# Performance work log

Measured on AMD Instinct MI355X. Metric: run time of the kernel, lower is better.

The kernel has to match this reference:

```python
import jax, jax.numpy as jnp
import numpy as np

NUM_HEAD = 12
D_MODEL = 768
SEQ_LEN = 4096
D_K = D_MODEL // NUM_HEAD
NEG = -1e9  # matches masked_fill(-1000000000.0)


def setup_inputs() -> dict:
    key = jax.random.key(0)
    ks = jax.random.split(key, 9)
    s = 1.0 / np.sqrt(D_MODEL)
    inp = {
        "x": jax.random.normal(ks[0], (1, SEQ_LEN, D_MODEL), jnp.float32),
        "Wq": jax.random.normal(ks[1], (D_MODEL, D_MODEL), jnp.float32) * s,
        "bq": jax.random.normal(ks[2], (D_MODEL,), jnp.float32) * 0.01,
        "Wk": jax.random.normal(ks[3], (D_MODEL, D_MODEL), jnp.float32) * s,
        "bk": jax.random.normal(ks[4], (D_MODEL,), jnp.float32) * 0.01,
        "Wv": jax.random.normal(ks[5], (D_MODEL, D_MODEL), jnp.float32) * s,
        "bv": jax.random.normal(ks[6], (D_MODEL,), jnp.float32) * 0.01,
        "Wo": jax.random.normal(ks[7], (D_MODEL, D_MODEL), jnp.float32) * s,
        "bo": jax.random.normal(ks[8], (D_MODEL,), jnp.float32) * 0.01,
    }
    return inp


def reference(x, Wq, bq, Wk, bk, Wv, bv, Wo, bo):
    # x: [B, S, D]. nn.Linear computes x @ W.T + b.
    B, S, D = x.shape

    def proj(W, b):
        y = jnp.einsum("bsd,ed->bse", x, W) + b
        # [B, S, H, d_k] -> [B, H, S, d_k]
        return y.reshape(B, S, NUM_HEAD, D_K).transpose(0, 2, 1, 3)

    q = proj(Wq, bq)
    k = proj(Wk, bk)
    v = proj(Wv, bv)

    scores = jnp.einsum("bhqd,bhkd->bhqk", q, k) / jnp.sqrt(
        jnp.asarray(D_K, x.dtype)
    )
    # causal (subsequent) mask: position q attends to k <= q
    causal = jnp.tril(jnp.ones((S, S), bool))
    scores = jnp.where(causal[None, None], scores, jnp.asarray(NEG, x.dtype))
    p_attn = jax.nn.softmax(scores, axis=-1)  # dropout is identity in eval
    ctx = jnp.einsum("bhqk,bhkd->bhqd", p_attn, v)
    ctx = ctx.transpose(0, 2, 1, 3).reshape(B, S, D)
    return jnp.einsum("bsd,ed->bse", ctx, Wo) + bo
```

## Files before the change

### kernel.cpp

```cpp
#include <hip/hip_runtime.h>

#define SEQ 4096
#define DM  768
#define NH  12
#define DK  64

typedef __bf16 bf16_t;
typedef bf16_t bf16x8 __attribute__((ext_vector_type(8)));
typedef bf16_t bf16x4 __attribute__((ext_vector_type(4)));
typedef float  f32x4  __attribute__((ext_vector_type(4)));
typedef short  s16x4  __attribute__((ext_vector_type(4)));

#define LOG2E 1.44269504088896340736f
#define SM_C  16.0f

static __device__ inline f32x4 mfma16x16x16_bf16(bf16x4 a, bf16x4 b, f32x4 c) {
#if __has_builtin(__builtin_amdgcn_mfma_f32_16x16x16_bf16)
    return __builtin_amdgcn_mfma_f32_16x16x16_bf16(a, b, c, 0, 0, 0);
#else
    return __builtin_amdgcn_mfma_f32_16x16x16bf16_1k(
        __builtin_bit_cast(s16x4, a), __builtin_bit_cast(s16x4, b), c, 0, 0, 0);
#endif
}

static __device__ __forceinline__ void gl_lds16(const bf16_t* g, bf16_t* l) {
    __builtin_amdgcn_global_load_lds(
        (const __attribute__((address_space(1))) void*)g,
        (__attribute__((address_space(3))) void*)l, 16, 0, 0);
}

__global__ __launch_bounds__(256) void cvt_bf16(
    const float* __restrict__ x,  const float* __restrict__ Wq,
    const float* __restrict__ Wk, const float* __restrict__ Wv,
    const float* __restrict__ Wo,
    bf16_t* __restrict__ xb, bf16_t* __restrict__ Wb)
{
    const int NXV = SEQ * DM / 4;
    const int NWV = DM * DM / 4;
    int i4 = blockIdx.x * 256 + threadIdx.x;
    const float* src; bf16_t* dst; int off;
    if (i4 < NXV) { src = x; dst = xb; off = i4; }
    else {
        int j = i4 - NXV;
        int w = j / NWV, jj = j - w * NWV;
        src = (w == 0) ? Wq : (w == 1) ? Wk : (w == 2) ? Wv : Wo;
        dst = Wb + (size_t)w * DM * DM;
        off = jj;
    }
    float4 v = *(const float4*)&src[(size_t)off * 4];
    bf16x4 t;
    t[0] = (bf16_t)v.x; t[1] = (bf16_t)v.y; t[2] = (bf16_t)v.z; t[3] = (bf16_t)v.w;
    *(bf16x4*)&dst[(size_t)off * 4] = t;
}

__global__ __launch_bounds__(256) void gemm_qkv2(
    const bf16_t* __restrict__ A, const bf16_t* __restrict__ Wb,
    const float* __restrict__ bq, const float* __restrict__ bk,
    const float* __restrict__ bv,
    bf16_t* __restrict__ Qb, bf16_t* __restrict__ Kb, bf16_t* __restrict__ Vbt)
{
    const int z = blockIdx.z;
    const bf16_t* W = Wb + (size_t)z * DM * DM;
    const float* bias = (z == 0) ? bq : (z == 1) ? bk : bv;

    __shared__ bf16_t As[128][64];
    __shared__ bf16_t Bs[128][64];

    const int tid  = threadIdx.x;
    const int wave = tid >> 6;
    const int lane = tid & 63;
    const int wm   = wave & 1, wn = wave >> 1;
    const int lrow = lane & 15;
    const int quad = lane >> 4;
    const int row0 = blockIdx.x * 128;
    const int col0 = blockIdx.y * 128;

    const int srow   = lane >> 3;
    const int schunk = (lane & 7) ^ srow;
    const int swz    = lrow & 7;

    f32x4 acc[4][4];
    #pragma unroll
    for (int i = 0; i < 4; i++)
        #pragma unroll
        for (int j = 0; j < 4; j++)
            acc[i][j] = (f32x4){0.f, 0.f, 0.f, 0.f};

    for (int k0 = 0; k0 < DM; k0 += 64) {
        __syncthreads();
        #pragma unroll
        for (int u = 0; u < 4; u++) {
            int R0 = wave * 32 + u * 8;
            gl_lds16(&A[(size_t)(row0 + R0 + srow) * DM + k0 + schunk * 8],
                     &As[R0][0]);
            gl_lds16(&W[(size_t)(col0 + R0 + srow) * DM + k0 + schunk * 8],
                     &Bs[R0][0]);
        }
        __syncthreads();

        #pragma unroll
        for (int s = 0; s < 2; s++) {
            bf16x8 af[4], bfr[4];
            #pragma unroll
            for (int mt = 0; mt < 4; mt++)
                af[mt] = *(const bf16x8*)
                    &As[wm * 64 + mt * 16 + lrow][(((s << 2) | quad) ^ swz) * 8];
            #pragma unroll
            for (int nt = 0; nt < 4; nt++)
                bfr[nt] = *(const bf16x8*)
                    &Bs[wn * 64 + nt * 16 + lrow][(((s << 2) | quad) ^ swz) * 8];
            #pragma unroll
            for (int mt = 0; mt < 4; mt++)
                #pragma unroll
                for (int nt = 0; nt < 4; nt++)
                    acc[mt][nt] = __builtin_amdgcn_mfma_f32_16x16x32_bf16(
                        af[mt], bfr[nt], acc[mt][nt], 0, 0, 0);
        }
    }

    if (z == 2) {
        #pragma unroll
        for (int nt = 0; nt < 4; nt++) {
            int col = col0 + wn * 64 + nt * 16 + lrow;
            float bvv = bias[col];
            #pragma unroll
            for (int mt = 0; mt < 4; mt++) {
                int row = row0 + wm * 64 + mt * 16 + quad * 4;
                bf16x4 t;
                #pragma unroll
                for (int r = 0; r < 4; r++) t[r] = (bf16_t)(acc[mt][nt][r] + bvv);
                *(bf16x4*)&Vbt[(size_t)col * SEQ + row] = t;
            }
        }
    } else {
        bf16_t* Cout = (z == 0) ? Qb : Kb;
        float scale = (z == 1) ? 0.125f : 1.0f;
        #pragma unroll
        for (int nt = 0; nt < 4; nt++) {
            int col = col0 + wn * 64 + nt * 16 + lrow;
            float bvv = bias[col];
            #pragma unroll
            for (int mt = 0; mt < 4; mt++) {
                #pragma unroll
                for (int r = 0; r < 4; r++) {
                    int row = row0 + wm * 64 + mt * 16 + quad * 4 + r;
                    Cout[(size_t)row * DM + col] =
                        (bf16_t)((acc[mt][nt][r] + bvv) * scale);
                }
            }
        }
    }
}

__global__ __launch_bounds__(256) void gemm_out2(
    const bf16_t* __restrict__ A, const bf16_t* __restrict__ W,
    const float* __restrict__ bias, float* __restrict__ C)
{
    __shared__ bf16_t As[128][64];
    __shared__ bf16_t Bs[64][64];

    const int tid  = threadIdx.x;
    const int wave = tid >> 6;
    const int lane = tid & 63;
    const int wm   = wave & 1, wn = wave >> 1;
    const int lrow = lane & 15;
    const int quad = lane >> 4;
    const int row0 = blockIdx.x * 128;
    const int col0 = blockIdx.y * 64;

    const int srow   = lane >> 3;
    const int schunk = (lane & 7) ^ srow;
    const int swz    = lrow & 7;

    f32x4 acc[4][2];
    #pragma unroll
    for (int i = 0; i < 4; i++)
        #pragma unroll
        for (int j = 0; j < 2; j++)
            acc[i][j] = (f32x4){0.f, 0.f, 0.f, 0.f};

    for (int k0 = 0; k0 < DM; k0 += 64) {
        __syncthreads();
        #pragma unroll
        for (int u = 0; u < 4; u++) {
            int R0 = wave * 32 + u * 8;
            gl_lds16(&A[(size_t)(row0 + R0 + srow) * DM + k0 + schunk * 8],
                     &As[R0][0]);
        }
        #pragma unroll
        for (int u = 0; u < 2; u++) {
            int R0 = wave * 16 + u * 8;
            gl_lds16(&W[(size_t)(col0 + R0 + srow) * DM + k0 + schunk * 8],
                     &Bs[R0][0]);
        }
        __syncthreads();

        #pragma unroll
        for (int s = 0; s < 2; s++) {
            bf16x8 af[4], bfr[2];
            #pragma unroll
            for (int mt = 0; mt < 4; mt++)
                af[mt] = *(const bf16x8*)
                    &As[wm * 64 + mt * 16 + lrow][(((s << 2) | quad) ^ swz) * 8];
            #pragma unroll
            for (int nt = 0; nt < 2; nt++)
                bfr[nt] = *(const bf16x8*)
                    &Bs[wn * 32 + nt * 16 + lrow][(((s << 2) | quad) ^ swz) * 8];
            #pragma unroll
            for (int mt = 0; mt < 4; mt++)
                #pragma unroll
                for (int nt = 0; nt < 2; nt++)
                    acc[mt][nt] = __builtin_amdgcn_mfma_f32_16x16x32_bf16(
                        af[mt], bfr[nt], acc[mt][nt], 0, 0, 0);
        }
    }

    #pragma unroll
    for (int nt = 0; nt < 2; nt++) {
        int col = col0 + wn * 32 + nt * 16 + lrow;
        float bvv = bias[col];
        #pragma unroll
        for (int mt = 0; mt < 4; mt++) {
            #pragma unroll
            for (int r = 0; r < 4; r++) {
                int row = row0 + wm * 64 + mt * 16 + quad * 4 + r;
                C[(size_t)row * DM + col] = acc[mt][nt][r] + bvv;
            }
        }
    }
}

__global__ __launch_bounds__(256) void flash_split2(
    const bf16_t* __restrict__ Qb, const bf16_t* __restrict__ Kb,
    const bf16_t* __restrict__ Vbt,
    float* __restrict__ Oacc ,
    float* __restrict__ Lacc )
{
    const int qi = blockIdx.x;
    const int s0 = blockIdx.y * 16;
    if (s0 > qi) return;
    const int h    = blockIdx.z;
    const int kend = min(s0 + 15, qi);
    const int tid  = threadIdx.x;
    const int wave = tid >> 6;
    const int lane = tid & 63;
    const int lrow = lane & 15;
    const int quad = lane >> 4;
    const int q0   = qi * 64;

    __shared__ bf16_t Ks[2][64][72];
    __shared__ bf16_t Vt[2][64][76];

    const int qrow = q0 + wave * 16 + lrow;
    bf16x8 qfrag[2];
    #pragma unroll
    for (int s = 0; s < 2; s++)
        qfrag[s] = *(const bf16x8*)&Qb[(size_t)qrow * DM + h * DK + s * 32 + quad * 8];

    f32x4 oT[4];
    #pragma unroll
    for (int dt = 0; dt < 4; dt++) oT[dt] = (f32x4){0.f, 0.f, 0.f, 0.f};
    float l_i = 0.f;

    const int r0 = tid >> 3;
    const int c0 = (tid & 7) * 8;
    const bf16_t* Kbase = Kb  + (size_t)h * DK + c0;
    const bf16_t* Vbase = Vbt + (size_t)(h * DK) * SEQ + c0;

    size_t ko = (size_t)s0 * 64;
    bf16x8 kr0 = *(const bf16x8*)&Kbase[(ko + r0)      * DM];
    bf16x8 kr1 = *(const bf16x8*)&Kbase[(ko + r0 + 32) * DM];
    bf16x8 vr0 = *(const bf16x8*)&Vbase[(size_t)(r0)      * SEQ + ko];
    bf16x8 vr1 = *(const bf16x8*)&Vbase[(size_t)(r0 + 32) * SEQ + ko];

    for (int kt = s0; kt <= kend; kt++) {
        const int b = kt & 1;
        *(bf16x8*)&Ks[b][r0][c0]      = kr0;
        *(bf16x8*)&Ks[b][r0 + 32][c0] = kr1;
        *(bf16x8*)&Vt[b][r0][c0]      = vr0;
        *(bf16x8*)&Vt[b][r0 + 32][c0] = vr1;
        __syncthreads();

        if (kt < kend) {
            size_t kn = (size_t)(kt + 1) * 64;
            kr0 = *(const bf16x8*)&Kbase[(kn + r0)      * DM];
            kr1 = *(const bf16x8*)&Kbase[(kn + r0 + 32) * DM];
            vr0 = *(const bf16x8*)&Vbase[(size_t)(r0)      * SEQ + kn];
            vr1 = *(const bf16x8*)&Vbase[(size_t)(r0 + 32) * SEQ + kn];
        }

        f32x4 sc[4];
        #pragma unroll
        for (int mt = 0; mt < 4; mt++) {
            f32x4 a = (f32x4){0.f, 0.f, 0.f, 0.f};
            #pragma unroll
            for (int s = 0; s < 2; s++) {
                bf16x8 kf = *(const bf16x8*)&Ks[b][mt * 16 + lrow][s * 32 + quad * 8];
                a = __builtin_amdgcn_mfma_f32_16x16x32_bf16(kf, qfrag[s], a, 0, 0, 0);
            }
            sc[mt] = a;
        }

        if (kt == qi) {
            int lq = wave * 16 + lrow;
            #pragma unroll
            for (int mt = 0; mt < 4; mt++)
                #pragma unroll
                for (int r = 0; r < 4; r++)
                    if (mt * 16 + quad * 4 + r > lq) sc[mt][r] = -1e30f;
        }

        bf16x4 pf[4];
        float rsum = 0.f;
        #pragma unroll
        for (int mt = 0; mt < 4; mt++) {
            bf16x4 t;
            #pragma unroll
            for (int r = 0; r < 4; r++) {
                float p = __builtin_amdgcn_exp2f((sc[mt][r] - SM_C) * LOG2E);
                rsum += p;
                t[r] = (bf16_t)p;
            }
            pf[mt] = t;
        }
        l_i += rsum;

        #pragma unroll
        for (int dt = 0; dt < 4; dt++)
            #pragma unroll
            for (int kb = 0; kb < 4; kb++) {
                bf16x4 vf = *(const bf16x4*)&Vt[b][dt * 16 + lrow][kb * 16 + quad * 4];
                oT[dt] = mfma16x16x16_bf16(vf, pf[kb], oT[dt]);
            }
    }

    #pragma unroll
    for (int dt = 0; dt < 4; dt++)
        #pragma unroll
        for (int r = 0; r < 4; r++) {
            int d = dt * 16 + quad * 4 + r;
            atomicAdd(&Oacc[((size_t)h * DK + d) * SEQ + q0 + wave * 16 + lrow],
                      oT[dt][r]);
        }
    l_i += __shfl_xor(l_i, 16, 64);
    l_i += __shfl_xor(l_i, 32, 64);
    if (quad == 0)
        atomicAdd(&Lacc[(size_t)h * SEQ + qrow], l_i);
}

__global__ __launch_bounds__(256) void ctx_epilogue(
    const float* __restrict__ Oacc, const float* __restrict__ Lacc,
    bf16_t* __restrict__ Ctx)
{
    const int qt = blockIdx.x;
    const int h  = blockIdx.y;
    const int tid = threadIdx.x;
    __shared__ float T[64][65];

    #pragma unroll
    for (int i = 0; i < 4; i++) {
        int v  = tid + i * 256;
        int d  = v >> 4;
        int qv = v & 15;
        f32x4 o4 = *(const f32x4*)&Oacc[((size_t)h * DK + d) * SEQ + qt * 64 + qv * 4];
        f32x4 l4 = *(const f32x4*)&Lacc[(size_t)h * SEQ + qt * 64 + qv * 4];
        #pragma unroll
        for (int j = 0; j < 4; j++)
            T[qv * 4 + j][d] = o4[j] / l4[j];
    }
    __syncthreads();
    #pragma unroll
    for (int i = 0; i < 2; i++) {
        int v  = tid + i * 256;
        int q  = v >> 3;
        int c8 = v & 7;
        bf16x8 t;
        #pragma unroll
        for (int j = 0; j < 8; j++)
            t[j] = (bf16_t)T[q][c8 * 8 + j];
        *(bf16x8*)&Ctx[(size_t)(qt * 64 + q) * DM + h * DK + c8 * 8] = t;
    }
}

extern "C" void kernel_launch(void* const* d_in, const int* in_sizes, int n_in,
                              void* d_out, int out_size, void* d_ws, size_t ws_size,
                              hipStream_t stream) {
    const float* x  = (const float*)d_in[0];
    const float* Wq = (const float*)d_in[1];
    const float* bq = (const float*)d_in[2];
    const float* Wk = (const float*)d_in[3];
    const float* bk = (const float*)d_in[4];
    const float* Wv = (const float*)d_in[5];
    const float* bv = (const float*)d_in[6];
    const float* Wo = (const float*)d_in[7];
    const float* bo = (const float*)d_in[8];
    float* out = (float*)d_out;

    const size_t NX = (size_t)SEQ * DM;
    const size_t NW = (size_t)DM * DM;

    bf16_t* xb   = (bf16_t*)d_ws;
    bf16_t* Qb   = xb  + NX;
    bf16_t* Kb   = Qb  + NX;
    bf16_t* Vbt  = Kb  + NX;
    bf16_t* Wb   = Vbt + NX;
    float*  Oacc = (float*)(Wb + 4 * NW);
    float*  Lacc = Oacc + NX;
    bf16_t* Cx   = xb;

    int cvt_blocks = (int)((NX + 4 * NW) / 4 / 256);
    cvt_bf16<<<cvt_blocks, 256, 0, stream>>>(x, Wq, Wk, Wv, Wo, xb, Wb);
    hipMemsetAsync(Oacc, 0, (NX + (size_t)NH * SEQ) * 4, stream);

    dim3 g1(SEQ / 128, DM / 128, 3);
    gemm_qkv2<<<g1, 256, 0, stream>>>(xb, Wb, bq, bk, bv, Qb, Kb, Vbt);

    dim3 g2(SEQ / 64, 4, NH);
    flash_split2<<<g2, 256, 0, stream>>>(Qb, Kb, Vbt, Oacc, Lacc);

    dim3 g3(SEQ / 64, NH);
    ctx_epilogue<<<g3, 256, 0, stream>>>(Oacc, Lacc, Cx);

    dim3 g4(SEQ / 128, DM / 64);
    gemm_out2<<<g4, 256, 0, stream>>>(Cx, Wb + 3 * NW, bo, out);
}
```

Baseline: 201.5 us.

## Use 128-row query tiles with 512 threads, compact causal grid and swizzled LDS

The flash kernel now processes 128 query rows per block with 8 waves, so each K/V tile loaded into LDS is shared by twice as many queries. A compact triangular block enumeration replaces the old grid and its early-exit blocks, and each block covers up to 8 key tiles. LDS padding is replaced by an XOR swizzle to avoid bank conflicts. The log2e factor is folded into the K scale so the exp2 argument needs no multiply. In exchange, per-wave causal skipping adds divergence, and the while-loop index decode costs some scalar work.

New measurement: 204.1 us. Within noise of the previous version (+1.3%).

```diff
diff --git a/kernel.cpp b/kernel.cpp
--- a/kernel.cpp
+++ b/kernel.cpp
@@ -12,7 +12,7 @@
 typedef short  s16x4  __attribute__((ext_vector_type(4)));
 
 #define LOG2E 1.44269504088896340736f
-#define SM_C  16.0f
+#define SM_C2 23.0831207f
 
 static __device__ inline f32x4 mfma16x16x16_bf16(bf16x4 a, bf16x4 b, f32x4 c) {
 #if __has_builtin(__builtin_amdgcn_mfma_f32_16x16x16_bf16)
@@ -134,7 +134,7 @@
         }
     } else {
         bf16_t* Cout = (z == 0) ? Qb : Kb;
-        float scale = (z == 1) ? 0.125f : 1.0f;
+        float scale = (z == 1) ? (0.125f * LOG2E) : 1.0f;
         #pragma unroll
         for (int nt = 0; nt < 4; nt++) {
             int col = col0 + wn * 64 + nt * 16 + lrow;
@@ -230,26 +230,33 @@
     }
 }
 
-__global__ __launch_bounds__(256) void flash_split2(
+__global__ __launch_bounds__(512) void flash_split3(
     const bf16_t* __restrict__ Qb, const bf16_t* __restrict__ Kb,
     const bf16_t* __restrict__ Vbt,
     float* __restrict__ Oacc ,
     float* __restrict__ Lacc )
 {
-    const int qi = blockIdx.x;
-    const int s0 = blockIdx.y * 16;
-    if (s0 > qi) return;
-    const int h    = blockIdx.z;
-    const int kend = min(s0 + 15, qi);
+    const int h = blockIdx.z;
+    const int f = blockIdx.x;
+    int g = 0;
+    while (f >= 2 * (g + 1) * (g + 2)) g++;
+    const int rem = f - 2 * g * (g + 1);
+    const int qs  = rem / (g + 1);
+    const int seg = rem - qs * (g + 1);
+    const int qi  = g * 4 + qs;
+    const int q0  = qi << 7;
+    const int kt0    = seg << 3;
+    const int ktlast = min(kt0 + 7, 2 * qi + 1);
+
     const int tid  = threadIdx.x;
     const int wave = tid >> 6;
     const int lane = tid & 63;
     const int lrow = lane & 15;
     const int quad = lane >> 4;
-    const int q0   = qi * 64;
-
-    __shared__ bf16_t Ks[2][64][72];
-    __shared__ bf16_t Vt[2][64][76];
+    const int swz  = lrow & 7;
+
+    __shared__ bf16_t Ks[2][64][64];
+    __shared__ bf16_t Vs[2][64][64];
 
     const int qrow = q0 + wave * 16 + lrow;
     bf16x8 qfrag[2];
@@ -262,32 +269,29 @@
     for (int dt = 0; dt < 4; dt++) oT[dt] = (f32x4){0.f, 0.f, 0.f, 0.f};
     float l_i = 0.f;
 
-    const int r0 = tid >> 3;
-    const int c0 = (tid & 7) * 8;
-    const bf16_t* Kbase = Kb  + (size_t)h * DK + c0;
-    const bf16_t* Vbase = Vbt + (size_t)(h * DK) * SEQ + c0;
-
-    size_t ko = (size_t)s0 * 64;
-    bf16x8 kr0 = *(const bf16x8*)&Kbase[(ko + r0)      * DM];
-    bf16x8 kr1 = *(const bf16x8*)&Kbase[(ko + r0 + 32) * DM];
-    bf16x8 vr0 = *(const bf16x8*)&Vbase[(size_t)(r0)      * SEQ + ko];
-    bf16x8 vr1 = *(const bf16x8*)&Vbase[(size_t)(r0 + 32) * SEQ + ko];
-
-    for (int kt = s0; kt <= kend; kt++) {
+    const int sr  = tid >> 3;
+    const int sc0 = tid & 7;
+    const int scn = sc0 ^ (sr & 7);
+    const bf16_t* Kbase = Kb  + (size_t)h * DK;
+    const bf16_t* Vbase = Vbt + (size_t)(h * DK) * SEQ;
+
+    size_t ko = (size_t)kt0 << 6;
+    bf16x8 kr = *(const bf16x8*)&Kbase[(ko + sr) * DM + sc0 * 8];
+    bf16x8 vr = *(const bf16x8*)&Vbase[(size_t)sr * SEQ + ko + sc0 * 8];
+
+    for (int kt = kt0; kt <= ktlast; kt++) {
         const int b = kt & 1;
-        *(bf16x8*)&Ks[b][r0][c0]      = kr0;
-        *(bf16x8*)&Ks[b][r0 + 32][c0] = kr1;
-        *(bf16x8*)&Vt[b][r0][c0]      = vr0;
-        *(bf16x8*)&Vt[b][r0 + 32][c0] = vr1;
+        *(bf16x8*)&Ks[b][sr][scn * 8] = kr;
+        *(bf16x8*)&Vs[b][sr][scn * 8] = vr;
         __syncthreads();
 
-        if (kt < kend) {
-            size_t kn = (size_t)(kt + 1) * 64;
-            kr0 = *(const bf16x8*)&Kbase[(kn + r0)      * DM];
-            kr1 = *(const bf16x8*)&Kbase[(kn + r0 + 32) * DM];
-            vr0 = *(const bf16x8*)&Vbase[(size_t)(r0)      * SEQ + kn];
-            vr1 = *(const bf16x8*)&Vbase[(size_t)(r0 + 32) * SEQ + kn];
-        }
+        if (kt < ktlast) {
+            size_t kn = (size_t)(kt + 1) << 6;
+            kr = *(const bf16x8*)&Kbase[(kn + sr) * DM + sc0 * 8];
+            vr = *(const bf16x8*)&Vbase[(size_t)sr * SEQ + kn + sc0 * 8];
+        }
+
+        if ((kt << 6) > q0 + wave * 16 + 15) continue;
 
         f32x4 sc[4];
         #pragma unroll
@@ -295,19 +299,20 @@
             f32x4 a = (f32x4){0.f, 0.f, 0.f, 0.f};
             #pragma unroll
             for (int s = 0; s < 2; s++) {
-                bf16x8 kf = *(const bf16x8*)&Ks[b][mt * 16 + lrow][s * 32 + quad * 8];
+                bf16x8 kf = *(const bf16x8*)
+                    &Ks[b][mt * 16 + lrow][((((s << 2) | quad)) ^ swz) * 8];
                 a = __builtin_amdgcn_mfma_f32_16x16x32_bf16(kf, qfrag[s], a, 0, 0, 0);
             }
             sc[mt] = a;
         }
 
-        if (kt == qi) {
-            int lq = wave * 16 + lrow;
+        if ((kt << 6) + 63 > q0 + wave * 16) {
             #pragma unroll
             for (int mt = 0; mt < 4; mt++)
                 #pragma unroll
-                for (int r = 0; r < 4; r++)
-                    if (mt * 16 + quad * 4 + r > lq) sc[mt][r] = -1e30f;
+                for (int rr = 0; rr < 4; rr++)
+                    if ((kt << 6) + mt * 16 + quad * 4 + rr > qrow)
+                        sc[mt][rr] = -1e30f;
         }
 
         bf16x4 pf[4];
@@ -316,10 +321,10 @@
         for (int mt = 0; mt < 4; mt++) {
             bf16x4 t;
             #pragma unroll
-            for (int r = 0; r < 4; r++) {
-                float p = __builtin_amdgcn_exp2f((sc[mt][r] - SM_C) * LOG2E);
+            for (int rr = 0; rr < 4; rr++) {
+                float p = __builtin_amdgcn_exp2f(sc[mt][rr] - SM_C2);
                 rsum += p;
-                t[r] = (bf16_t)p;
+                t[rr] = (bf16_t)p;
             }
             pf[mt] = t;
         }
@@ -329,7 +334,9 @@
         for (int dt = 0; dt < 4; dt++)
             #pragma unroll
             for (int kb = 0; kb < 4; kb++) {
-                bf16x4 vf = *(const bf16x4*)&Vt[b][dt * 16 + lrow][kb * 16 + quad * 4];
+                int c16 = (kb * 2 + (quad >> 1)) ^ swz;
+                bf16x4 vf = *(const bf16x4*)
+                    &Vs[b][dt * 16 + lrow][c16 * 8 + (quad & 1) * 4];
                 oT[dt] = mfma16x16x16_bf16(vf, pf[kb], oT[dt]);
             }
     }
@@ -337,10 +344,9 @@
     #pragma unroll
     for (int dt = 0; dt < 4; dt++)
         #pragma unroll
-        for (int r = 0; r < 4; r++) {
-            int d = dt * 16 + quad * 4 + r;
-            atomicAdd(&Oacc[((size_t)h * DK + d) * SEQ + q0 + wave * 16 + lrow],
-                      oT[dt][r]);
+        for (int rr = 0; rr < 4; rr++) {
+            int d = dt * 16 + quad * 4 + rr;
+            atomicAdd(&Oacc[((size_t)h * DK + d) * SEQ + qrow], oT[dt][rr]);
         }
     l_i += __shfl_xor(l_i, 16, 64);
     l_i += __shfl_xor(l_i, 32, 64);
@@ -415,8 +421,8 @@
     dim3 g1(SEQ / 128, DM / 128, 3);
     gemm_qkv2<<<g1, 256, 0, stream>>>(xb, Wb, bq, bk, bv, Qb, Kb, Vbt);
 
-    dim3 g2(SEQ / 64, 4, NH);
-    flash_split2<<<g2, 256, 0, stream>>>(Qb, Kb, Vbt, Oacc, Lacc);
+    dim3 g2(144, 1, NH);
+    flash_split3<<<g2, 512, 0, stream>>>(Qb, Kb, Vbt, Oacc, Lacc);
 
     dim3 g3(SEQ / 64, NH);
     ctx_epilogue<<<g3, 256, 0, stream>>>(Oacc, Lacc, Cx);
```
